# Kernel tuning notes

Hardware: AMD Instinct MI355X
Metric: run time of the kernel (lower is better)

Reference implementation:

```python
import jax, jax.numpy as jnp
import numpy as np

SUP_NUM = 2048
EPS_NORM = 1e-12
EPS_BN = 1e-5


def l2norm(v, axis):
    n = jnp.sqrt(jnp.sum(v * v, axis=axis, keepdims=True))
    return v / jnp.maximum(n, EPS_NORM)


def segment_mean(vals, ids, num_segments):
    # vals: [N, C], ids: [N] int -> [num_segments, C]
    s = jax.ops.segment_sum(vals, ids, num_segments=num_segments)
    cnt = jax.ops.segment_sum(jnp.ones((vals.shape[0],), vals.dtype), ids, num_segments=num_segments)
    return s / jnp.maximum(cnt, 1.0)[:, None]


def setup_inputs() -> dict:
    key = jax.random.key(0)
    ks = jax.random.split(key, 6)
    B, Cin, H, W = 1, 3, 1024, 1024
    Cf = 32
    x = jax.random.normal(ks[0], (B, Cin, H, W), dtype=jnp.float32)
    conv_feat = jax.random.normal(ks[1], (B, Cf, H, W), dtype=jnp.float32)
    vit_feature = jax.random.normal(ks[2], (B, SUP_NUM, Cf), dtype=jnp.float32)
    seg_ids = jax.random.randint(ks[3], (B * H * W,), 0, SUP_NUM, dtype=jnp.int32)
    w_soft = jax.random.normal(ks[4], (1, 2 * Cf, 3), dtype=jnp.float32) * 0.1
    b_soft = jnp.zeros((1,), jnp.float32)
    bn_gamma = jnp.ones((1,), jnp.float32)
    bn_beta = jnp.zeros((1,), jnp.float32)
    return {"x": x, "conv_feat": conv_feat, "vit_feature": vit_feature, "seg_ids": seg_ids,
            "w_soft": w_soft, "b_soft": b_soft, "bn_gamma": bn_gamma, "bn_beta": bn_beta}


def reference(x, conv_feat, vit_feature, seg_ids, w_soft, b_soft, bn_gamma, bn_beta):
    B, Cf, H, W = conv_feat.shape
    Cin = x.shape[1]
    # F.normalize(conv, p=2, dim=1)
    conv_1 = l2norm(conv_feat, axis=1)
    # [B,C,H,W] -> [B*H*W, C]
    F1 = conv_1.transpose(0, 2, 3, 1).reshape(-1, Cf)
    X = jax.lax.stop_gradient(x).transpose(0, 2, 3, 1).reshape(-1, Cin)
    # superpixel scatter-mean (replaces the per-segment Python loop)
    M_F = segment_mean(F1, seg_ids, SUP_NUM)                  # [Sup, Cf]
    X_F = segment_mean(X, seg_ids, SUP_NUM)                   # [Sup, Cin]
    M_F = M_F.reshape(B, SUP_NUM, Cf)
    X_F = X_F.reshape(B, SUP_NUM, Cin).transpose(0, 2, 1)     # [B, Cin, Sup]
    vit_n = l2norm(vit_feature, axis=-1)
    all_F = jnp.concatenate([M_F, vit_n], axis=-1).transpose(0, 2, 1)  # [B, 2Cf, Sup]
    all_F = l2norm(all_F, axis=1)
    # Conv1d(2Cf -> 1, k=3, pad=1)
    z = jax.lax.conv_general_dilated(all_F, w_soft, window_strides=(1,), padding=((1, 1),),
                                     dimension_numbers=("NCH", "OIH", "NCH")) + b_soft[None, :, None]
    # BatchNorm1d (training-mode batch stats over (B, L))
    mu = jnp.mean(z, axis=(0, 2), keepdims=True)
    var = jnp.mean((z - mu) ** 2, axis=(0, 2), keepdims=True)
    z = bn_gamma[None, :, None] * (z - mu) / jnp.sqrt(var + EPS_BN) + bn_beta[None, :, None]
    result = jax.nn.sigmoid(z)                                # [B, 1, Sup]
    gap = jnp.mean(result, axis=-1, keepdims=True)            # AdaptiveAvgPool1d(1)
    return (result, gap, all_F, X_F)
```

## Files before the change

### kernel.cpp

```cpp
#include <hip/hip_runtime.h>
#include <hip/hip_bf16.h>
#include <hip/hip_fp16.h>

#define SUP 2048
#define NXB 128
#define NG  6

#define S_CONV 2097152.0f
#define S_X    131072.0f
#define IS_CONV (1.0f/2097152.0f)
#define IS_X    (1.0f/131072.0f)

__global__ __launch_bounds__(256) void k_invnorm(const float* __restrict__ conv,
                                                 float* __restrict__ inv,
                                                 int npix) {
    int t = blockIdx.x * blockDim.x + threadIdx.x;
    int p = t * 4;
    if (p + 3 < npix) {
        float4 s = {0.f, 0.f, 0.f, 0.f};
#pragma unroll
        for (int c = 0; c < 32; ++c) {
            float4 v = *(const float4*)(conv + (size_t)c * npix + p);
            s.x += v.x * v.x; s.y += v.y * v.y; s.z += v.z * v.z; s.w += v.w * v.w;
        }
        float4 r;
        r.x = 1.0f / fmaxf(sqrtf(s.x), 1e-12f);
        r.y = 1.0f / fmaxf(sqrtf(s.y), 1e-12f);
        r.z = 1.0f / fmaxf(sqrtf(s.z), 1e-12f);
        r.w = 1.0f / fmaxf(sqrtf(s.w), 1e-12f);
        *(float4*)(inv + p) = r;
    } else {
        for (; p < npix; ++p) {
            float s = 0.f;
#pragma unroll
            for (int c = 0; c < 32; ++c) {
                float v = conv[(size_t)c * npix + p];
                s += v * v;
            }
            inv[p] = 1.0f / fmaxf(sqrtf(s), 1e-12f);
        }
    }
}

__global__ __launch_bounds__(512) void k_segacc(const float* __restrict__ conv,
                                                const float* __restrict__ x,
                                                const int* __restrict__ ids,
                                                const float* __restrict__ inv,
                                                float* __restrict__ accum,
                                                __half* __restrict__ pbuf,
                                                int npix) {
    __shared__ int sacc[6 * SUP];
    int g = blockIdx.y;
    for (int i = threadIdx.x; i < 6 * SUP; i += blockDim.x) sacc[i] = 0;
    __syncthreads();

    int per = ((npix + (int)gridDim.x - 1) / (int)gridDim.x + 3) & ~3;
    int start = blockIdx.x * per;
    int end = min(start + per, npix);
    int nvec = (end > start) ? ((end - start) & ~3) : 0;
    int vend = start + nvec;

    if (g < 5) {
        const float* c0 = conv + (size_t)g * 6 * npix;
        for (int p = start + (int)threadIdx.x * 4; p < vend; p += (int)blockDim.x * 4) {
            int4   s4 = *(const int4*)(ids + p);
            float4 w4 = *(const float4*)(inv + p);
#pragma unroll
            for (int c = 0; c < 6; ++c) {
                float4 v = *(const float4*)(c0 + (size_t)c * npix + p);
                atomicAdd(&sacc[c * SUP + s4.x], __float2int_rn(v.x * w4.x * S_CONV));
                atomicAdd(&sacc[c * SUP + s4.y], __float2int_rn(v.y * w4.y * S_CONV));
                atomicAdd(&sacc[c * SUP + s4.z], __float2int_rn(v.z * w4.z * S_CONV));
                atomicAdd(&sacc[c * SUP + s4.w], __float2int_rn(v.w * w4.w * S_CONV));
            }
        }
        for (int p = vend + (int)threadIdx.x; p < end; p += (int)blockDim.x) {
            int s = ids[p];
            float w = inv[p];
#pragma unroll
            for (int c = 0; c < 6; ++c)
                atomicAdd(&sacc[c * SUP + s],
                          __float2int_rn(c0[(size_t)c * npix + p] * w * S_CONV));
        }
    } else {
        const float* c30 = conv + (size_t)30 * npix;
        const float* c31 = conv + (size_t)31 * npix;
        for (int p = start + (int)threadIdx.x * 4; p < vend; p += (int)blockDim.x * 4) {
            int4   s4 = *(const int4*)(ids + p);
            float4 w4 = *(const float4*)(inv + p);
            float4 va = *(const float4*)(c30 + p);
            float4 vb = *(const float4*)(c31 + p);
            float4 a = *(const float4*)(x + p);
            float4 b = *(const float4*)(x + (size_t)npix + p);
            float4 c = *(const float4*)(x + (size_t)2 * npix + p);
            atomicAdd(&sacc[0 * SUP + s4.x], __float2int_rn(va.x * w4.x * S_CONV));
            atomicAdd(&sacc[0 * SUP + s4.y], __float2int_rn(va.y * w4.y * S_CONV));
            atomicAdd(&sacc[0 * SUP + s4.z], __float2int_rn(va.z * w4.z * S_CONV));
            atomicAdd(&sacc[0 * SUP + s4.w], __float2int_rn(va.w * w4.w * S_CONV));
            atomicAdd(&sacc[1 * SUP + s4.x], __float2int_rn(vb.x * w4.x * S_CONV));
            atomicAdd(&sacc[1 * SUP + s4.y], __float2int_rn(vb.y * w4.y * S_CONV));
            atomicAdd(&sacc[1 * SUP + s4.z], __float2int_rn(vb.z * w4.z * S_CONV));
            atomicAdd(&sacc[1 * SUP + s4.w], __float2int_rn(vb.w * w4.w * S_CONV));
            atomicAdd(&sacc[2 * SUP + s4.x], __float2int_rn(a.x * S_X));
            atomicAdd(&sacc[2 * SUP + s4.y], __float2int_rn(a.y * S_X));
            atomicAdd(&sacc[2 * SUP + s4.z], __float2int_rn(a.z * S_X));
            atomicAdd(&sacc[2 * SUP + s4.w], __float2int_rn(a.w * S_X));
            atomicAdd(&sacc[3 * SUP + s4.x], __float2int_rn(b.x * S_X));
            atomicAdd(&sacc[3 * SUP + s4.y], __float2int_rn(b.y * S_X));
            atomicAdd(&sacc[3 * SUP + s4.z], __float2int_rn(b.z * S_X));
            atomicAdd(&sacc[3 * SUP + s4.w], __float2int_rn(b.w * S_X));
            atomicAdd(&sacc[4 * SUP + s4.x], __float2int_rn(c.x * S_X));
            atomicAdd(&sacc[4 * SUP + s4.y], __float2int_rn(c.y * S_X));
            atomicAdd(&sacc[4 * SUP + s4.z], __float2int_rn(c.z * S_X));
            atomicAdd(&sacc[4 * SUP + s4.w], __float2int_rn(c.w * S_X));
            atomicAdd(&sacc[5 * SUP + s4.x], 1);
            atomicAdd(&sacc[5 * SUP + s4.y], 1);
            atomicAdd(&sacc[5 * SUP + s4.z], 1);
            atomicAdd(&sacc[5 * SUP + s4.w], 1);
        }
        for (int p = vend + (int)threadIdx.x; p < end; p += (int)blockDim.x) {
            int s = ids[p];
            float w = inv[p];
            atomicAdd(&sacc[0 * SUP + s], __float2int_rn(c30[p] * w * S_CONV));
            atomicAdd(&sacc[1 * SUP + s], __float2int_rn(c31[p] * w * S_CONV));
            atomicAdd(&sacc[2 * SUP + s], __float2int_rn(x[p] * S_X));
            atomicAdd(&sacc[3 * SUP + s], __float2int_rn(x[(size_t)npix + p] * S_X));
            atomicAdd(&sacc[4 * SUP + s], __float2int_rn(x[(size_t)2 * npix + p] * S_X));
            atomicAdd(&sacc[5 * SUP + s], 1);
        }
    }
    __syncthreads();

    int base = g * 6 * SUP;
    if (pbuf) {
        __half* dst = pbuf + (size_t)blockIdx.x * 36 * SUP + base;
        for (int i = threadIdx.x; i < 6 * SUP; i += blockDim.x) {
            int slot = i >> 11;
            float sc = (g < 5 || slot < 2) ? IS_CONV : (slot < 5 ? IS_X : 1.0f);
            dst[i] = __float2half((float)sacc[i] * sc);
        }
    } else {
        for (int i = threadIdx.x; i < 6 * SUP; i += blockDim.x) {
            int slot = i >> 11;
            float sc = (g < 5 || slot < 2) ? IS_CONV : (slot < 5 ? IS_X : 1.0f);
            unsafeAtomicAdd(&accum[base + i], (float)sacc[i] * sc);
        }
    }
}

__global__ __launch_bounds__(256) void k_reduce(const __half* __restrict__ pbuf,
                                                float* __restrict__ accum) {
    int j8 = (blockIdx.x * blockDim.x + threadIdx.x) * 8;
    if (j8 >= 36 * SUP) return;
    float s[8];
#pragma unroll
    for (int k = 0; k < 8; ++k) s[k] = 0.f;
    for (int b = 0; b < NXB; ++b) {
        uint4 u = *(const uint4*)(pbuf + (size_t)b * 36 * SUP + j8);
        __half2 h0 = *reinterpret_cast<__half2*>(&u.x);
        __half2 h1 = *reinterpret_cast<__half2*>(&u.y);
        __half2 h2 = *reinterpret_cast<__half2*>(&u.z);
        __half2 h3 = *reinterpret_cast<__half2*>(&u.w);
        float2 f0 = __half22float2(h0), f1 = __half22float2(h1);
        float2 f2 = __half22float2(h2), f3 = __half22float2(h3);
        s[0] += f0.x; s[1] += f0.y; s[2] += f1.x; s[3] += f1.y;
        s[4] += f2.x; s[5] += f2.y; s[6] += f3.x; s[7] += f3.y;
    }
    float4 o0 = {s[0], s[1], s[2], s[3]};
    float4 o1 = {s[4], s[5], s[6], s[7]};
    *(float4*)(accum + j8) = o0;
    *(float4*)(accum + j8 + 4) = o1;
}

__device__ __forceinline__ void compute_col(const float* __restrict__ accum,
                                            const float* __restrict__ vit,
                                            int g, float* __restrict__ col) {
    if (g < 0 || g >= SUP) {
#pragma unroll
        for (int c = 0; c < 64; ++c) col[c] = 0.f;
        return;
    }
    float cnt = fmaxf(accum[35 * SUP + g], 1.0f);
    float rc = 1.0f / cnt;
#pragma unroll
    for (int c = 0; c < 32; ++c) col[c] = accum[c * SUP + g] * rc;
    float vs = 0.f;
#pragma unroll
    for (int c = 0; c < 32; ++c) {
        float v = vit[g * 32 + c];
        col[32 + c] = v;
        vs += v * v;
    }
    float vinv = 1.0f / fmaxf(sqrtf(vs), 1e-12f);
#pragma unroll
    for (int c = 0; c < 32; ++c) col[32 + c] *= vinv;
    float ssq = 0.f;
#pragma unroll
    for (int c = 0; c < 64; ++c) ssq += col[c] * col[c];
    float ainv = 1.0f / fmaxf(sqrtf(ssq), 1e-12f);
#pragma unroll
    for (int c = 0; c < 64; ++c) col[c] *= ainv;
}

__global__ __launch_bounds__(256) void k_finalconv(const float* __restrict__ accum,
                                                   const float* __restrict__ vit,
                                                   const float* __restrict__ w,
                                                   const float* __restrict__ bias,
                                                   float* __restrict__ allF_out,
                                                   float* __restrict__ xf_out,
                                                   float* __restrict__ z_out) {
    __shared__ float L[258][65];
    __shared__ float sw[192];
    int t = threadIdx.x;
    int b0 = blockIdx.x * 256;
    if (t < 192) sw[t] = w[t];

    float col[64];
    int g = b0 + t;
    compute_col(accum, vit, g, col);
#pragma unroll
    for (int c = 0; c < 64; ++c) L[t + 1][c] = col[c];
#pragma unroll
    for (int c = 0; c < 64; ++c) allF_out[c * SUP + g] = col[c];
    {
        float cnt = fmaxf(accum[35 * SUP + g], 1.0f);
        float rc = 1.0f / cnt;
#pragma unroll
        for (int c = 0; c < 3; ++c)
            xf_out[c * SUP + g] = accum[(32 + c) * SUP + g] * rc;
    }
    if (t == 0) {
        compute_col(accum, vit, b0 - 1, col);
#pragma unroll
        for (int c = 0; c < 64; ++c) L[0][c] = col[c];
    }
    if (t == 255) {
        compute_col(accum, vit, b0 + 256, col);
#pragma unroll
        for (int c = 0; c < 64; ++c) L[257][c] = col[c];
    }
    __syncthreads();

    float acc = bias[0];
#pragma unroll
    for (int c = 0; c < 64; ++c) {
        acc += sw[c * 3] * L[t][c] + sw[c * 3 + 1] * L[t + 1][c]
             + sw[c * 3 + 2] * L[t + 2][c];
    }
    z_out[b0 + t] = acc;
}

__global__ __launch_bounds__(512) void k_head2(const float* __restrict__ z,
                                               const float* __restrict__ gamma,
                                               const float* __restrict__ beta,
                                               float* __restrict__ out) {
    __shared__ float red[8];
    __shared__ float bc[2];
    int tid = threadIdx.x;
    int lane = tid & 63, wid = tid >> 6;

    float zs[4];
#pragma unroll
    for (int j = 0; j < 4; ++j) zs[j] = z[j * 512 + tid];

    float s1 = zs[0] + zs[1] + zs[2] + zs[3];
#pragma unroll
    for (int o = 32; o > 0; o >>= 1) s1 += __shfl_down(s1, o);
    if (lane == 0) red[wid] = s1;
    __syncthreads();
    if (tid == 0) {
        float t = 0.f;
        for (int i = 0; i < 8; ++i) t += red[i];
        bc[0] = t / (float)SUP;
    }
    __syncthreads();
    float mu = bc[0];

    float s2 = 0.f;
#pragma unroll
    for (int j = 0; j < 4; ++j) { float d = zs[j] - mu; s2 += d * d; }
#pragma unroll
    for (int o = 32; o > 0; o >>= 1) s2 += __shfl_down(s2, o);
    __syncthreads();
    if (lane == 0) red[wid] = s2;
    __syncthreads();
    if (tid == 0) {
        float t = 0.f;
        for (int i = 0; i < 8; ++i) t += red[i];
        bc[1] = t / (float)SUP;
    }
    __syncthreads();
    float var = bc[1];

    float invstd = rsqrtf(var + 1e-5f);
    float gm = gamma[0], bt = beta[0];
    float gsum = 0.f;
#pragma unroll
    for (int j = 0; j < 4; ++j) {
        int p = j * 512 + tid;
        float zn = gm * (zs[j] - mu) * invstd + bt;
        float r = 1.0f / (1.0f + expf(-zn));
        out[p] = r;
        gsum += r;
    }
#pragma unroll
    for (int o = 32; o > 0; o >>= 1) gsum += __shfl_down(gsum, o);
    __syncthreads();
    if (lane == 0) red[wid] = gsum;
    __syncthreads();
    if (tid == 0) {
        float t = 0.f;
        for (int i = 0; i < 8; ++i) t += red[i];
        out[SUP] = t / (float)SUP;
    }
}

extern "C" void kernel_launch(void* const* d_in, const int* in_sizes, int n_in,
                              void* d_out, int out_size, void* d_ws, size_t ws_size,
                              hipStream_t stream) {
    const float* x     = (const float*)d_in[0];
    const float* conv  = (const float*)d_in[1];
    const float* vit   = (const float*)d_in[2];
    const int*   ids   = (const int*)d_in[3];
    const float* w     = (const float*)d_in[4];
    const float* b     = (const float*)d_in[5];
    const float* gamma = (const float*)d_in[6];
    const float* beta  = (const float*)d_in[7];
    float* out = (float*)d_out;

    int npix = in_sizes[3];

    float* inv = (float*)d_ws;
    float* accum = inv + npix;
    float* zbuf = accum + 36 * SUP;
    __half* pbuf = (__half*)(zbuf + SUP);

    size_t need = ((size_t)npix + 36 * SUP + SUP) * sizeof(float)
                + (size_t)NXB * 36 * SUP * sizeof(__half);
    bool useP = ws_size >= need;

    if (!useP) hipMemsetAsync(accum, 0, 36 * SUP * sizeof(float), stream);

    int nquad = (npix + 3) / 4;
    k_invnorm<<<(nquad + 255) / 256, 256, 0, stream>>>(conv, inv, npix);

    dim3 g2(NXB, NG);
    k_segacc<<<g2, 512, 0, stream>>>(conv, x, ids, inv, accum,
                                     useP ? pbuf : (__half*)nullptr, npix);
    if (useP) {
        k_reduce<<<(36 * SUP / 8 + 255) / 256, 256, 0, stream>>>(pbuf, accum);
    }

    float* allF = out + SUP + 1;
    float* xf = allF + 64 * SUP;
    k_finalconv<<<SUP / 256, 256, 0, stream>>>(accum, vit, w, b, allF, xf, zbuf);

    k_head2<<<1, 512, 0, stream>>>(zbuf, gamma, beta, out);
}
```

Before: 80.68 us.

## Pack two fixed-point channels per 32-bit LDS atomic and store inverse norms in fp16

Each shared-memory integer atomic now carries two 16-bit fixed-point channel sums (with borrow-correcting encoding), which halves the number of LDS atomics. The grid is restructured from 6 channel groups of 512 threads to 2 groups of 1024 threads, each covering 16 conv channels plus a packed x/count slot. The inverse-norm buffer is stored as fp16 to cut traffic. In exchange, the lower scales (1024, 512, 256) and 16-bit packing reduce precision and risk overflow of the packed low half when per-block segment sums grow large.

```diff
diff --git a/kernel.cpp b/kernel.cpp
--- a/kernel.cpp
+++ b/kernel.cpp
@@ -4,15 +4,23 @@
 
 #define SUP 2048
 #define NXB 128
-#define NG  6
-
-#define S_CONV 2097152.0f
-#define S_X    131072.0f
-#define IS_CONV (1.0f/2097152.0f)
-#define IS_X    (1.0f/131072.0f)
+
+#define SC_CONV 1024.0f
+#define SC_X0   512.0f
+#define SC_XLO  256.0f
+#define ISC_CONV (1.0f/1024.0f)
+#define ISC_X0   (1.0f/512.0f)
+#define ISC_XLO  (1.0f/256.0f)
+
+__device__ __forceinline__ int enc2i(int qa, int qb) {
+    return ((qa - (qb < 0 ? 1 : 0)) << 16) + (qb & 0xFFFF);
+}
+__device__ __forceinline__ int enc2f(float a, float b) {
+    return enc2i(__float2int_rn(a), __float2int_rn(b));
+}
 
 __global__ __launch_bounds__(256) void k_invnorm(const float* __restrict__ conv,
-                                                 float* __restrict__ inv,
+                                                 __half* __restrict__ inv,
                                                  int npix) {
     int t = blockIdx.x * blockDim.x + threadIdx.x;
     int p = t * 4;
@@ -23,12 +31,12 @@
             float4 v = *(const float4*)(conv + (size_t)c * npix + p);
             s.x += v.x * v.x; s.y += v.y * v.y; s.z += v.z * v.z; s.w += v.w * v.w;
         }
-        float4 r;
-        r.x = 1.0f / fmaxf(sqrtf(s.x), 1e-12f);
-        r.y = 1.0f / fmaxf(sqrtf(s.y), 1e-12f);
-        r.z = 1.0f / fmaxf(sqrtf(s.z), 1e-12f);
-        r.w = 1.0f / fmaxf(sqrtf(s.w), 1e-12f);
-        *(float4*)(inv + p) = r;
+        __half2 h0 = __floats2half2_rn(1.0f / fmaxf(sqrtf(s.x), 1e-12f),
+                                       1.0f / fmaxf(sqrtf(s.y), 1e-12f));
+        __half2 h1 = __floats2half2_rn(1.0f / fmaxf(sqrtf(s.z), 1e-12f),
+                                       1.0f / fmaxf(sqrtf(s.w), 1e-12f));
+        *(__half2*)(inv + p) = h0;
+        *(__half2*)(inv + p + 2) = h1;
     } else {
         for (; p < npix; ++p) {
             float s = 0.f;
@@ -37,21 +45,22 @@
                 float v = conv[(size_t)c * npix + p];
                 s += v * v;
             }
-            inv[p] = 1.0f / fmaxf(sqrtf(s), 1e-12f);
-        }
-    }
-}
-
-__global__ __launch_bounds__(512) void k_segacc(const float* __restrict__ conv,
-                                                const float* __restrict__ x,
-                                                const int* __restrict__ ids,
-                                                const float* __restrict__ inv,
-                                                float* __restrict__ accum,
-                                                __half* __restrict__ pbuf,
-                                                int npix) {
-    __shared__ int sacc[6 * SUP];
+            inv[p] = __float2half(1.0f / fmaxf(sqrtf(s), 1e-12f));
+        }
+    }
+}
+
+__global__ __launch_bounds__(1024) void k_segacc(const float* __restrict__ conv,
+                                                 const float* __restrict__ x,
+                                                 const int* __restrict__ ids,
+                                                 const __half* __restrict__ inv,
+                                                 float* __restrict__ accum,
+                                                 __half* __restrict__ pbuf,
+                                                 int npix) {
+    __shared__ int sacc[9 * SUP];
     int g = blockIdx.y;
-    for (int i = threadIdx.x; i < 6 * SUP; i += blockDim.x) sacc[i] = 0;
+    int cb = g * 16;
+    for (int i = threadIdx.x; i < 9 * SUP; i += blockDim.x) sacc[i] = 0;
     __syncthreads();
 
     int per = ((npix + (int)gridDim.x - 1) / (int)gridDim.x + 3) & ~3;
@@ -60,90 +69,86 @@
     int nvec = (end > start) ? ((end - start) & ~3) : 0;
     int vend = start + nvec;
 
-    if (g < 5) {
-        const float* c0 = conv + (size_t)g * 6 * npix;
-        for (int p = start + (int)threadIdx.x * 4; p < vend; p += (int)blockDim.x * 4) {
-            int4   s4 = *(const int4*)(ids + p);
-            float4 w4 = *(const float4*)(inv + p);
-#pragma unroll
-            for (int c = 0; c < 6; ++c) {
-                float4 v = *(const float4*)(c0 + (size_t)c * npix + p);
-                atomicAdd(&sacc[c * SUP + s4.x], __float2int_rn(v.x * w4.x * S_CONV));
-                atomicAdd(&sacc[c * SUP + s4.y], __float2int_rn(v.y * w4.y * S_CONV));
-                atomicAdd(&sacc[c * SUP + s4.z], __float2int_rn(v.z * w4.z * S_CONV));
-                atomicAdd(&sacc[c * SUP + s4.w], __float2int_rn(v.w * w4.w * S_CONV));
-            }
-        }
-        for (int p = vend + (int)threadIdx.x; p < end; p += (int)blockDim.x) {
-            int s = ids[p];
-            float w = inv[p];
-#pragma unroll
-            for (int c = 0; c < 6; ++c)
-                atomicAdd(&sacc[c * SUP + s],
-                          __float2int_rn(c0[(size_t)c * npix + p] * w * S_CONV));
-        }
-    } else {
-        const float* c30 = conv + (size_t)30 * npix;
-        const float* c31 = conv + (size_t)31 * npix;
-        for (int p = start + (int)threadIdx.x * 4; p < vend; p += (int)blockDim.x * 4) {
-            int4   s4 = *(const int4*)(ids + p);
-            float4 w4 = *(const float4*)(inv + p);
-            float4 va = *(const float4*)(c30 + p);
-            float4 vb = *(const float4*)(c31 + p);
+    const float* cc = conv + (size_t)cb * npix;
+
+    for (int p = start + (int)threadIdx.x * 4; p < vend; p += (int)blockDim.x * 4) {
+        int4 s4 = *(const int4*)(ids + p);
+        __half2 h01 = *(const __half2*)(inv + p);
+        __half2 h23 = *(const __half2*)(inv + p + 2);
+        float w0 = __low2float(h01), w1 = __high2float(h01);
+        float w2 = __low2float(h23), w3 = __high2float(h23);
+#pragma unroll
+        for (int cp = 0; cp < 8; ++cp) {
+            float4 va = *(const float4*)(cc + (size_t)(2 * cp) * npix + p);
+            float4 vb = *(const float4*)(cc + (size_t)(2 * cp + 1) * npix + p);
+            atomicAdd(&sacc[cp * SUP + s4.x], enc2f(va.x * w0 * SC_CONV, vb.x * w0 * SC_CONV));
+            atomicAdd(&sacc[cp * SUP + s4.y], enc2f(va.y * w1 * SC_CONV, vb.y * w1 * SC_CONV));
+            atomicAdd(&sacc[cp * SUP + s4.z], enc2f(va.z * w2 * SC_CONV, vb.z * w2 * SC_CONV));
+            atomicAdd(&sacc[cp * SUP + s4.w], enc2f(va.w * w3 * SC_CONV, vb.w * w3 * SC_CONV));
+        }
+        if (g == 0) {
             float4 a = *(const float4*)(x + p);
             float4 b = *(const float4*)(x + (size_t)npix + p);
+            atomicAdd(&sacc[8 * SUP + s4.x], enc2f(a.x * SC_X0, b.x * SC_XLO));
+            atomicAdd(&sacc[8 * SUP + s4.y], enc2f(a.y * SC_X0, b.y * SC_XLO));
+            atomicAdd(&sacc[8 * SUP + s4.z], enc2f(a.z * SC_X0, b.z * SC_XLO));
+            atomicAdd(&sacc[8 * SUP + s4.w], enc2f(a.w * SC_X0, b.w * SC_XLO));
+        } else {
             float4 c = *(const float4*)(x + (size_t)2 * npix + p);
-            atomicAdd(&sacc[0 * SUP + s4.x], __float2int_rn(va.x * w4.x * S_CONV));
-            atomicAdd(&sacc[0 * SUP + s4.y], __float2int_rn(va.y * w4.y * S_CONV));
-            atomicAdd(&sacc[0 * SUP + s4.z], __float2int_rn(va.z * w4.z * S_CONV));
-            atomicAdd(&sacc[0 * SUP + s4.w], __float2int_rn(va.w * w4.w * S_CONV));
-            atomicAdd(&sacc[1 * SUP + s4.x], __float2int_rn(vb.x * w4.x * S_CONV));
-            atomicAdd(&sacc[1 * SUP + s4.y], __float2int_rn(vb.y * w4.y * S_CONV));
-            atomicAdd(&sacc[1 * SUP + s4.z], __float2int_rn(vb.z * w4.z * S_CONV));
-            atomicAdd(&sacc[1 * SUP + s4.w], __float2int_rn(vb.w * w4.w * S_CONV));
-            atomicAdd(&sacc[2 * SUP + s4.x], __float2int_rn(a.x * S_X));
-            atomicAdd(&sacc[2 * SUP + s4.y], __float2int_rn(a.y * S_X));
-            atomicAdd(&sacc[2 * SUP + s4.z], __float2int_rn(a.z * S_X));
-            atomicAdd(&sacc[2 * SUP + s4.w], __float2int_rn(a.w * S_X));
-            atomicAdd(&sacc[3 * SUP + s4.x], __float2int_rn(b.x * S_X));
-            atomicAdd(&sacc[3 * SUP + s4.y], __float2int_rn(b.y * S_X));
-            atomicAdd(&sacc[3 * SUP + s4.z], __float2int_rn(b.z * S_X));
-            atomicAdd(&sacc[3 * SUP + s4.w], __float2int_rn(b.w * S_X));
-            atomicAdd(&sacc[4 * SUP + s4.x], __float2int_rn(c.x * S_X));
-            atomicAdd(&sacc[4 * SUP + s4.y], __float2int_rn(c.y * S_X));
-            atomicAdd(&sacc[4 * SUP + s4.z], __float2int_rn(c.z * S_X));
-            atomicAdd(&sacc[4 * SUP + s4.w], __float2int_rn(c.w * S_X));
-            atomicAdd(&sacc[5 * SUP + s4.x], 1);
-            atomicAdd(&sacc[5 * SUP + s4.y], 1);
-            atomicAdd(&sacc[5 * SUP + s4.z], 1);
-            atomicAdd(&sacc[5 * SUP + s4.w], 1);
-        }
-        for (int p = vend + (int)threadIdx.x; p < end; p += (int)blockDim.x) {
-            int s = ids[p];
-            float w = inv[p];
-            atomicAdd(&sacc[0 * SUP + s], __float2int_rn(c30[p] * w * S_CONV));
-            atomicAdd(&sacc[1 * SUP + s], __float2int_rn(c31[p] * w * S_CONV));
-            atomicAdd(&sacc[2 * SUP + s], __float2int_rn(x[p] * S_X));
-            atomicAdd(&sacc[3 * SUP + s], __float2int_rn(x[(size_t)npix + p] * S_X));
-            atomicAdd(&sacc[4 * SUP + s], __float2int_rn(x[(size_t)2 * npix + p] * S_X));
-            atomicAdd(&sacc[5 * SUP + s], 1);
-        }
-    }
-    __syncthreads();
-
-    int base = g * 6 * SUP;
-    if (pbuf) {
-        __half* dst = pbuf + (size_t)blockIdx.x * 36 * SUP + base;
-        for (int i = threadIdx.x; i < 6 * SUP; i += blockDim.x) {
-            int slot = i >> 11;
-            float sc = (g < 5 || slot < 2) ? IS_CONV : (slot < 5 ? IS_X : 1.0f);
-            dst[i] = __float2half((float)sacc[i] * sc);
-        }
-    } else {
-        for (int i = threadIdx.x; i < 6 * SUP; i += blockDim.x) {
-            int slot = i >> 11;
-            float sc = (g < 5 || slot < 2) ? IS_CONV : (slot < 5 ? IS_X : 1.0f);
-            unsafeAtomicAdd(&accum[base + i], (float)sacc[i] * sc);
+            atomicAdd(&sacc[8 * SUP + s4.x], enc2i(1, __float2int_rn(c.x * SC_XLO)));
+            atomicAdd(&sacc[8 * SUP + s4.y], enc2i(1, __float2int_rn(c.y * SC_XLO)));
+            atomicAdd(&sacc[8 * SUP + s4.z], enc2i(1, __float2int_rn(c.z * SC_XLO)));
+            atomicAdd(&sacc[8 * SUP + s4.w], enc2i(1, __float2int_rn(c.w * SC_XLO)));
+        }
+    }
+    for (int p = vend + (int)threadIdx.x; p < end; p += (int)blockDim.x) {
+        int s = ids[p];
+        float w = __half2float(inv[p]);
+#pragma unroll
+        for (int cp = 0; cp < 8; ++cp) {
+            float va = cc[(size_t)(2 * cp) * npix + p];
+            float vb = cc[(size_t)(2 * cp + 1) * npix + p];
+            atomicAdd(&sacc[cp * SUP + s], enc2f(va * w * SC_CONV, vb * w * SC_CONV));
+        }
+        if (g == 0) {
+            atomicAdd(&sacc[8 * SUP + s],
+                      enc2f(x[p] * SC_X0, x[(size_t)npix + p] * SC_XLO));
+        } else {
+            atomicAdd(&sacc[8 * SUP + s],
+                      enc2i(1, __float2int_rn(x[(size_t)2 * npix + p] * SC_XLO)));
+        }
+    }
+    __syncthreads();
+
+    for (int i = threadIdx.x; i < 9 * SUP; i += blockDim.x) {
+        int S = sacc[i];
+        int qb = (int)(short)(S & 0xFFFF);
+        int qa = (S - qb) >> 16;
+        int row = i >> 11;
+        int s = i & (SUP - 1);
+        int hi_row, lo_row;
+        float fhi, flo;
+        if (row < 8) {
+            int ch = cb + 2 * row;
+            hi_row = ch; lo_row = ch + 1;
+            fhi = (float)qa * ISC_CONV;
+            flo = (float)qb * ISC_CONV;
+        } else if (g == 0) {
+            hi_row = 32; lo_row = 33;
+            fhi = (float)qa * ISC_X0;
+            flo = (float)qb * ISC_XLO;
+        } else {
+            hi_row = 35; lo_row = 34;
+            fhi = (float)qa;
+            flo = (float)qb * ISC_XLO;
+        }
+        if (pbuf) {
+            __half* dst = pbuf + (size_t)blockIdx.x * 36 * SUP;
+            dst[hi_row * SUP + s] = __float2half(fhi);
+            dst[lo_row * SUP + s] = __float2half(flo);
+        } else {
+            unsafeAtomicAdd(&accum[hi_row * SUP + s], fhi);
+            unsafeAtomicAdd(&accum[lo_row * SUP + s], flo);
         }
     }
 }
@@ -330,12 +335,12 @@
 
     int npix = in_sizes[3];
 
-    float* inv = (float*)d_ws;
-    float* accum = inv + npix;
+    __half* inv = (__half*)d_ws;
+    float* accum = (float*)((char*)d_ws + ((size_t)npix * 2 + 255 & ~(size_t)255));
     float* zbuf = accum + 36 * SUP;
     __half* pbuf = (__half*)(zbuf + SUP);
 
-    size_t need = ((size_t)npix + 36 * SUP + SUP) * sizeof(float)
+    size_t need = ((size_t)npix * 2 + 256) + (36 * SUP + SUP) * sizeof(float)
                 + (size_t)NXB * 36 * SUP * sizeof(__half);
     bool useP = ws_size >= need;
 
@@ -344,9 +349,9 @@
     int nquad = (npix + 3) / 4;
     k_invnorm<<<(nquad + 255) / 256, 256, 0, stream>>>(conv, inv, npix);
 
-    dim3 g2(NXB, NG);
-    k_segacc<<<g2, 512, 0, stream>>>(conv, x, ids, inv, accum,
-                                     useP ? pbuf : (__half*)nullptr, npix);
+    dim3 g2(NXB, 2);
+    k_segacc<<<g2, 1024, 0, stream>>>(conv, x, ids, inv, accum,
+                                      useP ? pbuf : (__half*)nullptr, npix);
     if (useP) {
         k_reduce<<<(36 * SUP / 8 + 255) / 256, 256, 0, stream>>>(pbuf, accum);
     }
```

After: 80.98 us. No clear change (+0.4%).
